# Performance work log

Hardware: AMD Instinct MI355X
Metric: run time of the kernel (lower is better)

The kernel has to match this reference:

```python
import jax, jax.numpy as jnp
import numpy as np

N_NODES = 50000
N_EDGES = 640000
IN, HID, OUT = 128, 128, 40


def _sage_conv(x, src, dst, W_l, b_l, W_r, num_nodes):
    """PyG SAGEConv (aggr='mean', root_weight=True):
       out_i = mean_{j in N(i)} x_j @ W_l^T + b_l + x_i @ W_r^T
    """
    msgs = x[src]  # [E, d] gather over source nodes
    agg = jax.ops.segment_sum(msgs, dst, num_segments=num_nodes)  # [N, d]
    deg = jax.ops.segment_sum(jnp.ones((src.shape[0],), x.dtype), dst,
                              num_segments=num_nodes)  # [N]
    mean = agg / jnp.maximum(deg, 1.0)[:, None]
    return mean @ W_l.T + b_l + x @ W_r.T


def setup_inputs() -> dict:
    key = jax.random.key(0)
    ks = jax.random.split(key, 12)
    x = jax.random.normal(ks[0], (N_NODES, IN), dtype=jnp.float32)
    edge_index = jax.random.randint(ks[1], (2, N_EDGES), 0, N_NODES, dtype=jnp.int64)

    def lin(k, fan_out, fan_in):
        s = 1.0 / np.sqrt(fan_in)
        return jax.random.uniform(k, (fan_out, fan_in), jnp.float32, -s, s)

    return {
        "x": x,
        "edge_index": edge_index,
        "W1l": lin(ks[2], HID, IN),  "b1": jnp.zeros((HID,), jnp.float32), "W1r": lin(ks[3], HID, IN),
        "W2l": lin(ks[4], HID, HID), "b2": jnp.zeros((HID,), jnp.float32), "W2r": lin(ks[5], HID, HID),
        "W3l": lin(ks[6], OUT, HID), "b3": jnp.zeros((OUT,), jnp.float32), "W3r": lin(ks[7], OUT, HID),
    }


def reference(x, edge_index, W1l, b1, W1r, W2l, b2, W2r, W3l, b3, W3r):
    src, dst = edge_index[0], edge_index[1]
    n = x.shape[0]
    # Dropout is identity in eval mode; reference is the deterministic forward.
    h = _sage_conv(x, src, dst, W1l, b1, W1r, n)
    h = jax.nn.relu(h)
    h = _sage_conv(h, src, dst, W2l, b2, W2r, n)
    h = jax.nn.relu(h)
    h = _sage_conv(h, src, dst, W3l, b3, W3r, n)
    return jax.nn.log_softmax(h, axis=-1)
```

## Files before the change

### kernel.cpp

```cpp
#include <hip/hip_runtime.h>

#define NN 50000
#define NE 640000
#define NBUCK 196
#define NSB 157
#define EPB 4096
#define EPT 16
#define COLCAP 8192
#define FDIM 128
#define FOUT 40

typedef unsigned int uint;
typedef unsigned short ushort;
typedef unsigned char uchar;
typedef __attribute__((ext_vector_type(8))) __bf16 bf16x8;
typedef __attribute__((ext_vector_type(4))) float f32x4;
typedef __attribute__((ext_vector_type(2))) float f32x2;

union BF8 { bf16x8 v; uint4 u; ushort s[8]; };

__device__ __forceinline__ ushort f2bf(float f){
  uint b = __float_as_uint(f);
  b += 0x7fffu + ((b >> 16) & 1u);
  return (ushort)(b >> 16);
}
__device__ __forceinline__ float bflo(uint v){ return __uint_as_float(v << 16); }
__device__ __forceinline__ float bfhi(uint v){ return __uint_as_float(v & 0xffff0000u); }
__device__ __forceinline__ uint pack2(float a, float b){
  return (uint)f2bf(a) | ((uint)f2bf(b) << 16);
}
__device__ __forceinline__ int get_edge(const void* ep, int is64, int idx){
  return is64 ? (int)(((const long long*)ep)[idx]) : ((const int*)ep)[idx];
}

__device__ __forceinline__ uint fp8enc(float f){
  uint b = __float_as_uint(f);
  uint s = (b >> 24) & 0x80u;
  float af = __uint_as_float(b & 0x7fffffffu);
  if(af < 0.015625f){
    uint m = (uint)__float2int_rn(af * 512.0f);
    return (m == 8u) ? (s | 0x08u) : (s | m);
  }
  uint ab = __float_as_uint(af);
  ab += 0x7ffffu + ((ab >> 20) & 1u);
  int e = (int)(ab >> 23) - 120;
  uint m = (ab >> 20) & 7u;
  if(e > 15){ e = 15; m = 6u; }
  return s | ((uint)e << 3) | m;
}
__device__ __forceinline__ float fp8dec(uint byte){
  uint s = (byte & 0x80u) << 24;
  uint e = (byte >> 3) & 15u;
  uint m = byte & 7u;
  float nrm = __uint_as_float(s | ((e + 120u) << 23) | (m << 20));
  float den = __uint_as_float(s | __float_as_uint((float)m * 0.001953125f));
  return e ? nrm : den;
}
__device__ __forceinline__ void fp8add4(uint dw, float* a){
#if __has_builtin(__builtin_amdgcn_cvt_pk_f32_fp8)
  f32x2 p0 = __builtin_amdgcn_cvt_pk_f32_fp8((int)dw, false);
  f32x2 p1 = __builtin_amdgcn_cvt_pk_f32_fp8((int)dw, true);
  a[0] += p0[0]; a[1] += p0[1]; a[2] += p1[0]; a[3] += p1[1];
#else
  a[0] += fp8dec(dw & 0xffu);
  a[1] += fp8dec((dw >> 8) & 0xffu);
  a[2] += fp8dec((dw >> 16) & 0xffu);
  a[3] += fp8dec(dw >> 24);
#endif
}

__launch_bounds__(256)
__global__ void k_pre(const float* __restrict__ x,
                      const float* __restrict__ W1l, const float* __restrict__ W1r,
                      const float* __restrict__ b1,
                      uchar* __restrict__ u8, ushort* __restrict__ v,
                      const unsigned long long* __restrict__ e64,
                      int* __restrict__ flag){
  if(blockIdx.x >= 625){
    if(threadIdx.x < 64){
      unsigned long long vv = e64[threadIdx.x];
      int ok = (int)__all(vv < 4294967296ULL);
      if(threadIdx.x == 0) *flag = ok;
    }
    return;
  }
  int g = threadIdx.x >> 6;
  int l = threadIdx.x & 63;
  int worker = blockIdx.x;
  int r16 = l & 15, q = l >> 4;

  BF8 bl[2][4], br[2][4];
#pragma unroll
  for(int tt = 0; tt < 2; ++tt){
    int colw = 32 * g + 16 * tt + r16;
    const float* pl = W1l + colw * FDIM + q * 8;
    const float* pr = W1r + colw * FDIM + q * 8;
#pragma unroll
    for(int ks = 0; ks < 4; ++ks){
      float4 x0 = *(const float4*)(pl + 32 * ks);
      float4 x1 = *(const float4*)(pl + 32 * ks + 4);
      BF8 t;
      t.s[0]=f2bf(x0.x); t.s[1]=f2bf(x0.y); t.s[2]=f2bf(x0.z); t.s[3]=f2bf(x0.w);
      t.s[4]=f2bf(x1.x); t.s[5]=f2bf(x1.y); t.s[6]=f2bf(x1.z); t.s[7]=f2bf(x1.w);
      bl[tt][ks] = t;
      float4 y0 = *(const float4*)(pr + 32 * ks);
      float4 y1 = *(const float4*)(pr + 32 * ks + 4);
      BF8 w;
      w.s[0]=f2bf(y0.x); w.s[1]=f2bf(y0.y); w.s[2]=f2bf(y0.z); w.s[3]=f2bf(y0.w);
      w.s[4]=f2bf(y1.x); w.s[5]=f2bf(y1.y); w.s[6]=f2bf(y1.z); w.s[7]=f2bf(y1.w);
      br[tt][ks] = w;
    }
  }
  float bv0 = b1[32 * g + r16];
  float bv1 = b1[32 * g + 16 + r16];

  for(int s = 0; s < 5; ++s){
    int m0 = (worker * 5 + s) * 16;
    BF8 a[4];
    const float* pf = x + (size_t)(m0 + r16) * FDIM + q * 8;
#pragma unroll
    for(int ks = 0; ks < 4; ++ks){
      float4 x0 = *(const float4*)(pf + 32 * ks);
      float4 x1 = *(const float4*)(pf + 32 * ks + 4);
      BF8 t;
      t.s[0]=f2bf(x0.x); t.s[1]=f2bf(x0.y); t.s[2]=f2bf(x0.z); t.s[3]=f2bf(x0.w);
      t.s[4]=f2bf(x1.x); t.s[5]=f2bf(x1.y); t.s[6]=f2bf(x1.z); t.s[7]=f2bf(x1.w);
      a[ks] = t;
    }
    f32x4 aU0 = {0,0,0,0}, aU1 = {0,0,0,0}, aV0 = {0,0,0,0}, aV1 = {0,0,0,0};
#pragma unroll
    for(int ks = 0; ks < 4; ++ks){
      aU0 = __builtin_amdgcn_mfma_f32_16x16x32_bf16(a[ks].v, bl[0][ks].v, aU0, 0, 0, 0);
      aV0 = __builtin_amdgcn_mfma_f32_16x16x32_bf16(a[ks].v, br[0][ks].v, aV0, 0, 0, 0);
      aU1 = __builtin_amdgcn_mfma_f32_16x16x32_bf16(a[ks].v, bl[1][ks].v, aU1, 0, 0, 0);
      aV1 = __builtin_amdgcn_mfma_f32_16x16x32_bf16(a[ks].v, br[1][ks].v, aV1, 0, 0, 0);
    }
#pragma unroll
    for(int r = 0; r < 4; ++r){
      size_t row = (size_t)(m0 + q * 4 + r);
      u8[row * FDIM + 32 * g + r16]      = (uchar)fp8enc(aU0[r]);
      u8[row * FDIM + 32 * g + 16 + r16] = (uchar)fp8enc(aU1[r]);
      v[row * FDIM + 32 * g + r16]       = f2bf(aV0[r] + bv0);
      v[row * FDIM + 32 * g + 16 + r16]  = f2bf(aV1[r] + bv1);
    }
  }
}

__global__ void k_hist(const void* __restrict__ edges, const int* __restrict__ flag,
                       int* __restrict__ bh){
  __shared__ int cnt[NBUCK];
  int t = threadIdx.x, sb = blockIdx.x;
  for(int i = t; i < NBUCK; i += 256) cnt[i] = 0;
  __syncthreads();
  int is64 = *flag;
  int e0 = sb * EPB + t;
#pragma unroll
  for(int i = 0; i < EPT; ++i){
    int e = e0 + i * 256;
    if(e < NE){
      int d = get_edge(edges, is64, NE + e);
      atomicAdd(&cnt[d >> 8], 1);
    }
  }
  __syncthreads();
  for(int i = t; i < NBUCK; i += 256) bh[i * NSB + sb] = cnt[i];
}

__global__ void k_bscan(int* __restrict__ bh, int* __restrict__ bases){
  __shared__ int s[256];
  int t = threadIdx.x;
  int tot = 0;
  if(t < NBUCK){
    const int* row = bh + t * NSB;
#pragma unroll 4
    for(int i = 0; i < NSB; ++i) tot += row[i];
  }
  s[t] = tot; __syncthreads();
  for(int o = 1; o < 256; o <<= 1){
    int a = (t >= o) ? s[t - o] : 0;
    __syncthreads(); s[t] += a; __syncthreads();
  }
  int base = s[t] - tot;
  if(t < NBUCK){
    bases[t] = base;
    int* row = bh + t * NSB;
    int run = base;
    for(int i = 0; i < NSB; ++i){ int vv = row[i]; row[i] = run; run += vv; }
  }
  if(t == 0) bases[NBUCK] = NE;
}

__launch_bounds__(256)
__global__ void k_scatter(const void* __restrict__ edges, const int* __restrict__ flag,
                          const int* __restrict__ bh, uint* __restrict__ recbuf){
  __shared__ int cnt[NBUCK], off[NBUCK], cur[NBUCK], gbase[NBUCK];
  __shared__ int s[256];
  __shared__ int nTot_s;
  __shared__ uint recLds[EPB];
  int t = threadIdx.x, sb = blockIdx.x;
  for(int i = t; i < NBUCK; i += 256) cnt[i] = 0;
  __syncthreads();
  int is64 = *flag;
  uint recs[EPT];
  int e0 = sb * EPB + t;
#pragma unroll
  for(int i = 0; i < EPT; ++i){
    int e = e0 + i * 256;
    if(e < NE){
      uint sn = (uint)get_edge(edges, is64, e);
      uint d  = (uint)get_edge(edges, is64, NE + e);
      recs[i] = (d << 16) | sn;
      atomicAdd(&cnt[d >> 8], 1);
    } else recs[i] = 0xFFFFFFFFu;
  }
  __syncthreads();
  int v = (t < NBUCK) ? cnt[t] : 0;
  s[t] = v; __syncthreads();
  for(int o = 1; o < 256; o <<= 1){
    int a = (t >= o) ? s[t - o] : 0;
    __syncthreads(); s[t] += a; __syncthreads();
  }
  if(t < NBUCK){ off[t] = s[t] - v; cur[t] = 0; gbase[t] = bh[t * NSB + sb]; }
  if(t == 255) nTot_s = s[255];
  __syncthreads();
#pragma unroll
  for(int i = 0; i < EPT; ++i){
    uint r = recs[i];
    if(r != 0xFFFFFFFFu){
      int b = (int)(r >> 24);
      int q = off[b] + atomicAdd(&cur[b], 1);
      recLds[q] = r;
    }
  }
  __syncthreads();
  int nTot = nTot_s;
  for(int q = t; q < nTot; q += 256){
    uint r = recLds[q];
    int b = (int)(r >> 24);
    recbuf[gbase[b] + (q - off[b])] = r;
  }
}

__global__ void k_csr(const uint* __restrict__ recbuf, const int* __restrict__ bases,
                      int* __restrict__ rp, int* __restrict__ col){
  __shared__ int cnt[256], rpl[256], cur[256];
  __shared__ int s[256];
  __shared__ int colL[COLCAP];
  int t = threadIdx.x, b = blockIdx.x;
  int base = bases[b], n = bases[b + 1] - base;
  cnt[t] = 0; __syncthreads();
  for(int q = t; q < n; q += 256) atomicAdd(&cnt[(recbuf[base + q] >> 16) & 255], 1);
  __syncthreads();
  int v = cnt[t];
  s[t] = v; __syncthreads();
  for(int o = 1; o < 256; o <<= 1){
    int a = (t >= o) ? s[t - o] : 0;
    __syncthreads(); s[t] += a; __syncthreads();
  }
  rpl[t] = s[t] - v; cur[t] = 0;
  int node = b * 256 + t;
  if(node < NN) rp[node] = base + rpl[t];
  if(b == 0 && t == 0) rp[NN] = NE;
  __syncthreads();
  if(n <= COLCAP){
    for(int q = t; q < n; q += 256){
      uint r = recbuf[base + q];
      int dl = (r >> 16) & 255;
      int p = rpl[dl] + atomicAdd(&cur[dl], 1);
      colL[p] = (int)(r & 0xFFFFu);
    }
    __syncthreads();
    for(int q = t; q < n; q += 256) col[base + q] = colL[q];
  } else {
    for(int q = t; q < n; q += 256){
      uint r = recbuf[base + q];
      int dl = (r >> 16) & 255;
      int p = rpl[dl] + atomicAdd(&cur[dl], 1);
      col[base + p] = (int)(r & 0xFFFFu);
    }
  }
}

__global__ void k_aggv8(const uchar* __restrict__ u8, const ushort* __restrict__ v,
                        const int* __restrict__ rp, const int* __restrict__ col,
                        ushort* __restrict__ h){
  int node = (blockIdx.x * blockDim.x + threadIdx.x) >> 6;
  if(node >= NN) return;
  int l = threadIdx.x & 63;
  int c8 = l & 7, eg = l >> 3;
  int beg = rp[node], deg = rp[node + 1] - beg;
  float acc[16];
#pragma unroll
  for(int i = 0; i < 16; ++i) acc[i] = 0.f;
  const uchar* fbase = u8 + c8 * 16;

  for(int base = 0; base < deg; base += 64){
    int nchunk = min(deg - base, 64);
    int idx = col[beg + base + min(l, nchunk - 1)];
#pragma unroll 2
    for(int j = 0; j < nchunk; j += 8){
      int e = j + eg;
      int s = __shfl(idx, min(e, nchunk - 1));
      uint4 w = *(const uint4*)(fbase + (size_t)s * FDIM);
      if(e < nchunk){
        fp8add4(w.x, acc + 0);
        fp8add4(w.y, acc + 4);
        fp8add4(w.z, acc + 8);
        fp8add4(w.w, acc + 12);
      }
    }
  }
#pragma unroll
  for(int i = 0; i < 16; ++i){
    acc[i] += __shfl_xor(acc[i], 8);
    acc[i] += __shfl_xor(acc[i], 16);
    acc[i] += __shfl_xor(acc[i], 32);
  }
  if(eg == 0){
    float inv = 1.0f / (float)max(deg, 1);
    const ushort* pv = v + (size_t)node * FDIM + c8 * 16;
    uint4 v0 = *(const uint4*)(pv);
    uint4 v1 = *(const uint4*)(pv + 8);
    uint4 o0, o1;
    o0.x = pack2(fmaxf(acc[0]*inv  + bflo(v0.x), 0.f), fmaxf(acc[1]*inv  + bfhi(v0.x), 0.f));
    o0.y = pack2(fmaxf(acc[2]*inv  + bflo(v0.y), 0.f), fmaxf(acc[3]*inv  + bfhi(v0.y), 0.f));
    o0.z = pack2(fmaxf(acc[4]*inv  + bflo(v0.z), 0.f), fmaxf(acc[5]*inv  + bfhi(v0.z), 0.f));
    o0.w = pack2(fmaxf(acc[6]*inv  + bflo(v0.w), 0.f), fmaxf(acc[7]*inv  + bfhi(v0.w), 0.f));
    o1.x = pack2(fmaxf(acc[8]*inv  + bflo(v1.x), 0.f), fmaxf(acc[9]*inv  + bfhi(v1.x), 0.f));
    o1.y = pack2(fmaxf(acc[10]*inv + bflo(v1.y), 0.f), fmaxf(acc[11]*inv + bfhi(v1.y), 0.f));
    o1.z = pack2(fmaxf(acc[12]*inv + bflo(v1.z), 0.f), fmaxf(acc[13]*inv + bfhi(v1.z), 0.f));
    o1.w = pack2(fmaxf(acc[14]*inv + bflo(v1.w), 0.f), fmaxf(acc[15]*inv + bfhi(v1.w), 0.f));
    ushort* ph = h + (size_t)node * FDIM + c8 * 16;
    *(uint4*)(ph)     = o0;
    *(uint4*)(ph + 8) = o1;
  }
}

__launch_bounds__(256)
__global__ void k_linuv2(const ushort* __restrict__ inB,
                         const float* __restrict__ Wl, const float* __restrict__ Wr,
                         const float* __restrict__ bias,
                         uchar* __restrict__ u8, ushort* __restrict__ v){
  int g = threadIdx.x >> 6;
  int l = threadIdx.x & 63;
  int worker = blockIdx.x;
  int r16 = l & 15, q = l >> 4;

  BF8 bl[2][4], br[2][4];
#pragma unroll
  for(int tt = 0; tt < 2; ++tt){
    int colw = 32 * g + 16 * tt + r16;
    const float* pl = Wl + colw * FDIM + q * 8;
    const float* pr = Wr + colw * FDIM + q * 8;
#pragma unroll
    for(int ks = 0; ks < 4; ++ks){
      float4 x0 = *(const float4*)(pl + 32 * ks);
      float4 x1 = *(const float4*)(pl + 32 * ks + 4);
      BF8 t;
      t.s[0]=f2bf(x0.x); t.s[1]=f2bf(x0.y); t.s[2]=f2bf(x0.z); t.s[3]=f2bf(x0.w);
      t.s[4]=f2bf(x1.x); t.s[5]=f2bf(x1.y); t.s[6]=f2bf(x1.z); t.s[7]=f2bf(x1.w);
      bl[tt][ks] = t;
      float4 y0 = *(const float4*)(pr + 32 * ks);
      float4 y1 = *(const float4*)(pr + 32 * ks + 4);
      BF8 w;
      w.s[0]=f2bf(y0.x); w.s[1]=f2bf(y0.y); w.s[2]=f2bf(y0.z); w.s[3]=f2bf(y0.w);
      w.s[4]=f2bf(y1.x); w.s[5]=f2bf(y1.y); w.s[6]=f2bf(y1.z); w.s[7]=f2bf(y1.w);
      br[tt][ks] = w;
    }
  }
  float bv0 = bias[32 * g + r16];
  float bv1 = bias[32 * g + 16 + r16];

  for(int s = 0; s < 5; ++s){
    int m0 = (worker * 5 + s) * 16;
    BF8 a[4];
    const ushort* pb = inB + (size_t)(m0 + r16) * FDIM + q * 8;
#pragma unroll
    for(int ks = 0; ks < 4; ++ks) a[ks].u = *(const uint4*)(pb + 32 * ks);
    f32x4 aU0 = {0,0,0,0}, aU1 = {0,0,0,0}, aV0 = {0,0,0,0}, aV1 = {0,0,0,0};
#pragma unroll
    for(int ks = 0; ks < 4; ++ks){
      aU0 = __builtin_amdgcn_mfma_f32_16x16x32_bf16(a[ks].v, bl[0][ks].v, aU0, 0, 0, 0);
      aV0 = __builtin_amdgcn_mfma_f32_16x16x32_bf16(a[ks].v, br[0][ks].v, aV0, 0, 0, 0);
      aU1 = __builtin_amdgcn_mfma_f32_16x16x32_bf16(a[ks].v, bl[1][ks].v, aU1, 0, 0, 0);
      aV1 = __builtin_amdgcn_mfma_f32_16x16x32_bf16(a[ks].v, br[1][ks].v, aV1, 0, 0, 0);
    }
#pragma unroll
    for(int r = 0; r < 4; ++r){
      size_t row = (size_t)(m0 + q * 4 + r);
      u8[row * FDIM + 32 * g + r16]      = (uchar)fp8enc(aU0[r]);
      u8[row * FDIM + 32 * g + 16 + r16] = (uchar)fp8enc(aU1[r]);
      v[row * FDIM + 32 * g + r16]       = f2bf(aV0[r] + bv0);
      v[row * FDIM + 32 * g + 16 + r16]  = f2bf(aV1[r] + bv1);
    }
  }
}

__launch_bounds__(192)
__global__ void k_linuv40(const ushort* __restrict__ inB,
                          const float* __restrict__ Wl, const float* __restrict__ Wr,
                          const float* __restrict__ bias,
                          ushort* __restrict__ u3, ushort* __restrict__ v3){
  int g = threadIdx.x >> 6;
  int l = threadIdx.x & 63;
  int worker = blockIdx.x;
  int r16 = l & 15, q = l >> 4;
  int colw = 16 * g + r16;
  bool vcol = colw < FOUT;

  BF8 bl[4], br[4];
#pragma unroll
  for(int ks = 0; ks < 4; ++ks){
    BF8 t, w;
    if(vcol){
      const float* pl = Wl + colw * FDIM + q * 8 + 32 * ks;
      const float* pr = Wr + colw * FDIM + q * 8 + 32 * ks;
      float4 x0 = ((const float4*)pl)[0], x1 = ((const float4*)pl)[1];
      t.s[0]=f2bf(x0.x); t.s[1]=f2bf(x0.y); t.s[2]=f2bf(x0.z); t.s[3]=f2bf(x0.w);
      t.s[4]=f2bf(x1.x); t.s[5]=f2bf(x1.y); t.s[6]=f2bf(x1.z); t.s[7]=f2bf(x1.w);
      float4 y0 = ((const float4*)pr)[0], y1 = ((const float4*)pr)[1];
      w.s[0]=f2bf(y0.x); w.s[1]=f2bf(y0.y); w.s[2]=f2bf(y0.z); w.s[3]=f2bf(y0.w);
      w.s[4]=f2bf(y1.x); w.s[5]=f2bf(y1.y); w.s[6]=f2bf(y1.z); w.s[7]=f2bf(y1.w);
    } else {
      t.u = make_uint4(0,0,0,0);
      w.u = make_uint4(0,0,0,0);
    }
    bl[ks] = t; br[ks] = w;
  }
  float bv = vcol ? bias[colw] : 0.f;

  for(int s = 0; s < 5; ++s){
    int m0 = (worker * 5 + s) * 16;
    BF8 a[4];
    const ushort* pb = inB + (size_t)(m0 + r16) * FDIM + q * 8;
#pragma unroll
    for(int ks = 0; ks < 4; ++ks) a[ks].u = *(const uint4*)(pb + 32 * ks);
    f32x4 aU = {0,0,0,0}, aV = {0,0,0,0};
#pragma unroll
    for(int ks = 0; ks < 4; ++ks){
      aU = __builtin_amdgcn_mfma_f32_16x16x32_bf16(a[ks].v, bl[ks].v, aU, 0, 0, 0);
      aV = __builtin_amdgcn_mfma_f32_16x16x32_bf16(a[ks].v, br[ks].v, aV, 0, 0, 0);
    }
    if(vcol){
#pragma unroll
      for(int r = 0; r < 4; ++r){
        size_t row = (size_t)(m0 + q * 4 + r);
        u3[row * FOUT + colw] = f2bf(aU[r]);
        v3[row * FOUT + colw] = f2bf(aV[r] + bv);
      }
    }
  }
}

__global__ void k_agg40(const ushort* __restrict__ u3, const ushort* __restrict__ v3,
                        const int* __restrict__ rp, const int* __restrict__ col,
                        float* __restrict__ out){
  int node = (blockIdx.x * blockDim.x + threadIdx.x) >> 6;
  if(node >= NN) return;
  int l = threadIdx.x & 63;
  int c = l % 20, sl = l / 20;
  const ushort* fbase = u3 + 2 * c;

  int beg = rp[node], deg = rp[node + 1] - beg;
  float a0 = 0.f, a1 = 0.f;
  for(int base = 0; base < deg; base += 60){
    int nchunk = min(deg - base, 60);
    int idx = col[beg + base + min(l, nchunk - 1)];
#pragma unroll 2
    for(int j = 0; j < nchunk; j += 3){
      int e = j + sl;
      int s = __shfl(idx, min(e, nchunk - 1));
      uint w = *(const uint*)(fbase + (size_t)s * FOUT);
      if(sl < 3 && e < nchunk){
        a0 += bflo(w); a1 += bfhi(w);
      }
    }
  }
  a0 += __shfl(a0, l + 20) + __shfl(a0, l + 40);
  a1 += __shfl(a1, l + 20) + __shfl(a1, l + 40);

  float inv = 1.0f / (float)max(deg, 1);
  float z0 = 0.f, z1 = 0.f;
  if(l < 20){
    uint vv = *(const uint*)(v3 + (size_t)node * FOUT + 2 * c);
    z0 = a0 * inv + bflo(vv);
    z1 = a1 * inv + bfhi(vv);
  }
  float m = (l < 20) ? fmaxf(z0, z1) : -1e30f;
#pragma unroll
  for(int d = 1; d < 64; d <<= 1) m = fmaxf(m, __shfl_xor(m, d));
  float es = (l < 20) ? (__expf(z0 - m) + __expf(z1 - m)) : 0.f;
#pragma unroll
  for(int d = 1; d < 64; d <<= 1) es += __shfl_xor(es, d);
  float lse = m + __logf(es);
  if(l < 20){
    *(float2*)(out + (size_t)node * FOUT + 2 * c) = make_float2(z0 - lse, z1 - lse);
  }
}

extern "C" void kernel_launch(void* const* d_in, const int* in_sizes, int n_in,
                              void* d_out, int out_size, void* d_ws, size_t ws_size,
                              hipStream_t stream){
  const float* x   = (const float*)d_in[0];
  const void*  edges = d_in[1];
  const float* W1l = (const float*)d_in[2];
  const float* b1  = (const float*)d_in[3];
  const float* W1r = (const float*)d_in[4];
  const float* W2l = (const float*)d_in[5];
  const float* b2  = (const float*)d_in[6];
  const float* W2r = (const float*)d_in[7];
  const float* W3l = (const float*)d_in[8];
  const float* b3  = (const float*)d_in[9];
  const float* W3r = (const float*)d_in[10];
  float* out = (float*)d_out;

  char* ws = (char*)d_ws;
  size_t off = 0;
  auto alloc = [&](size_t bytes)->void*{
    void* p = ws + off;
    off += (bytes + 255) & ~(size_t)255;
    return p;
  };
  ushort* u    = (ushort*)alloc((size_t)NN * FDIM * 2);
  ushort* v    = (ushort*)alloc((size_t)NN * FDIM * 2);
  ushort* h    = (ushort*)alloc((size_t)NN * FDIM * 2);
  ushort* h2   = (ushort*)alloc((size_t)NN * FDIM * 2);
  int*    rp   = (int*)alloc((size_t)(NN + 1) * 4);
  int*    col  = (int*)alloc((size_t)NE * 4);
  uint*   recbuf = (uint*)alloc((size_t)NE * 4);
  int*    bh   = (int*)alloc((size_t)NBUCK * NSB * 4);
  int*    bases= (int*)alloc((size_t)(NBUCK + 1) * 4);
  int*    flag = (int*)alloc(256);
  uchar*  u8   = (uchar*)u;

  int aggGrid = (NN * 64 + 255) / 256;
  k_pre<<<626, 256, 0, stream>>>(x, W1l, W1r, b1, u8, v,
                                 (const unsigned long long*)edges, flag);
  k_hist<<<NSB, 256, 0, stream>>>(edges, flag, bh);
  k_bscan<<<1, 256, 0, stream>>>(bh, bases);
  k_scatter<<<NSB, 256, 0, stream>>>(edges, flag, bh, recbuf);
  k_csr<<<NBUCK, 256, 0, stream>>>(recbuf, bases, rp, col);

  k_aggv8<<<aggGrid, 256, 0, stream>>>(u8, v, rp, col, h);
  k_linuv2<<<625, 256, 0, stream>>>(h, W2l, W2r, b2, u8, v);
  k_aggv8<<<aggGrid, 256, 0, stream>>>(u8, v, rp, col, h2);
  k_linuv40<<<625, 192, 0, stream>>>(h2, W3l, W3r, b3, u, v);
  k_agg40<<<aggGrid, 256, 0, stream>>>(u, v, rp, col, out);
}
```

Baseline: 214.7 us.

## Replace histogram+scan CSR build with fixed-capacity buckets and atomic offsets

```diff
diff --git a/kernel.cpp b/kernel.cpp
--- a/kernel.cpp
+++ b/kernel.cpp
@@ -6,7 +6,7 @@
 #define NSB 157
 #define EPB 4096
 #define EPT 16
-#define COLCAP 8192
+#define BCAP 4096
 #define FDIM 128
 #define FOUT 40
 
@@ -75,18 +75,19 @@
                       const float* __restrict__ b1,
                       uchar* __restrict__ u8, ushort* __restrict__ v,
                       const unsigned long long* __restrict__ e64,
-                      int* __restrict__ flag){
-  if(blockIdx.x >= 625){
-    if(threadIdx.x < 64){
-      unsigned long long vv = e64[threadIdx.x];
+                      int* __restrict__ flag, int* __restrict__ gcur){
+  if(blockIdx.x >= 3125){
+    int t = threadIdx.x;
+    if(t < NBUCK) gcur[t] = 0;
+    if(t < 64){
+      unsigned long long vv = e64[t];
       int ok = (int)__all(vv < 4294967296ULL);
-      if(threadIdx.x == 0) *flag = ok;
+      if(t == 0) *flag = ok;
     }
     return;
   }
   int g = threadIdx.x >> 6;
   int l = threadIdx.x & 63;
-  int worker = blockIdx.x;
   int r16 = l & 15, q = l >> 4;
 
   BF8 bl[2][4], br[2][4];
@@ -114,86 +115,40 @@
   float bv0 = b1[32 * g + r16];
   float bv1 = b1[32 * g + 16 + r16];
 
-  for(int s = 0; s < 5; ++s){
-    int m0 = (worker * 5 + s) * 16;
-    BF8 a[4];
-    const float* pf = x + (size_t)(m0 + r16) * FDIM + q * 8;
-#pragma unroll
-    for(int ks = 0; ks < 4; ++ks){
-      float4 x0 = *(const float4*)(pf + 32 * ks);
-      float4 x1 = *(const float4*)(pf + 32 * ks + 4);
-      BF8 t;
-      t.s[0]=f2bf(x0.x); t.s[1]=f2bf(x0.y); t.s[2]=f2bf(x0.z); t.s[3]=f2bf(x0.w);
-      t.s[4]=f2bf(x1.x); t.s[5]=f2bf(x1.y); t.s[6]=f2bf(x1.z); t.s[7]=f2bf(x1.w);
-      a[ks] = t;
-    }
-    f32x4 aU0 = {0,0,0,0}, aU1 = {0,0,0,0}, aV0 = {0,0,0,0}, aV1 = {0,0,0,0};
-#pragma unroll
-    for(int ks = 0; ks < 4; ++ks){
-      aU0 = __builtin_amdgcn_mfma_f32_16x16x32_bf16(a[ks].v, bl[0][ks].v, aU0, 0, 0, 0);
-      aV0 = __builtin_amdgcn_mfma_f32_16x16x32_bf16(a[ks].v, br[0][ks].v, aV0, 0, 0, 0);
-      aU1 = __builtin_amdgcn_mfma_f32_16x16x32_bf16(a[ks].v, bl[1][ks].v, aU1, 0, 0, 0);
-      aV1 = __builtin_amdgcn_mfma_f32_16x16x32_bf16(a[ks].v, br[1][ks].v, aV1, 0, 0, 0);
-    }
-#pragma unroll
-    for(int r = 0; r < 4; ++r){
-      size_t row = (size_t)(m0 + q * 4 + r);
-      u8[row * FDIM + 32 * g + r16]      = (uchar)fp8enc(aU0[r]);
-      u8[row * FDIM + 32 * g + 16 + r16] = (uchar)fp8enc(aU1[r]);
-      v[row * FDIM + 32 * g + r16]       = f2bf(aV0[r] + bv0);
-      v[row * FDIM + 32 * g + 16 + r16]  = f2bf(aV1[r] + bv1);
-    }
-  }
-}
-
-__global__ void k_hist(const void* __restrict__ edges, const int* __restrict__ flag,
-                       int* __restrict__ bh){
-  __shared__ int cnt[NBUCK];
-  int t = threadIdx.x, sb = blockIdx.x;
-  for(int i = t; i < NBUCK; i += 256) cnt[i] = 0;
-  __syncthreads();
-  int is64 = *flag;
-  int e0 = sb * EPB + t;
-#pragma unroll
-  for(int i = 0; i < EPT; ++i){
-    int e = e0 + i * 256;
-    if(e < NE){
-      int d = get_edge(edges, is64, NE + e);
-      atomicAdd(&cnt[d >> 8], 1);
-    }
-  }
-  __syncthreads();
-  for(int i = t; i < NBUCK; i += 256) bh[i * NSB + sb] = cnt[i];
-}
-
-__global__ void k_bscan(int* __restrict__ bh, int* __restrict__ bases){
-  __shared__ int s[256];
-  int t = threadIdx.x;
-  int tot = 0;
-  if(t < NBUCK){
-    const int* row = bh + t * NSB;
-#pragma unroll 4
-    for(int i = 0; i < NSB; ++i) tot += row[i];
-  }
-  s[t] = tot; __syncthreads();
-  for(int o = 1; o < 256; o <<= 1){
-    int a = (t >= o) ? s[t - o] : 0;
-    __syncthreads(); s[t] += a; __syncthreads();
-  }
-  int base = s[t] - tot;
-  if(t < NBUCK){
-    bases[t] = base;
-    int* row = bh + t * NSB;
-    int run = base;
-    for(int i = 0; i < NSB; ++i){ int vv = row[i]; row[i] = run; run += vv; }
-  }
-  if(t == 0) bases[NBUCK] = NE;
+  int m0 = blockIdx.x * 16;
+  BF8 a[4];
+  const float* pf = x + (size_t)(m0 + r16) * FDIM + q * 8;
+#pragma unroll
+  for(int ks = 0; ks < 4; ++ks){
+    float4 x0 = *(const float4*)(pf + 32 * ks);
+    float4 x1 = *(const float4*)(pf + 32 * ks + 4);
+    BF8 t;
+    t.s[0]=f2bf(x0.x); t.s[1]=f2bf(x0.y); t.s[2]=f2bf(x0.z); t.s[3]=f2bf(x0.w);
+    t.s[4]=f2bf(x1.x); t.s[5]=f2bf(x1.y); t.s[6]=f2bf(x1.z); t.s[7]=f2bf(x1.w);
+    a[ks] = t;
+  }
+  f32x4 aU0 = {0,0,0,0}, aU1 = {0,0,0,0}, aV0 = {0,0,0,0}, aV1 = {0,0,0,0};
+#pragma unroll
+  for(int ks = 0; ks < 4; ++ks){
+    aU0 = __builtin_amdgcn_mfma_f32_16x16x32_bf16(a[ks].v, bl[0][ks].v, aU0, 0, 0, 0);
+    aV0 = __builtin_amdgcn_mfma_f32_16x16x32_bf16(a[ks].v, br[0][ks].v, aV0, 0, 0, 0);
+    aU1 = __builtin_amdgcn_mfma_f32_16x16x32_bf16(a[ks].v, bl[1][ks].v, aU1, 0, 0, 0);
+    aV1 = __builtin_amdgcn_mfma_f32_16x16x32_bf16(a[ks].v, br[1][ks].v, aV1, 0, 0, 0);
+  }
+#pragma unroll
+  for(int r = 0; r < 4; ++r){
+    size_t row = (size_t)(m0 + q * 4 + r);
+    u8[row * FDIM + 32 * g + r16]      = (uchar)fp8enc(aU0[r]);
+    u8[row * FDIM + 32 * g + 16 + r16] = (uchar)fp8enc(aU1[r]);
+    v[row * FDIM + 32 * g + r16]       = f2bf(aV0[r] + bv0);
+    v[row * FDIM + 32 * g + 16 + r16]  = f2bf(aV1[r] + bv1);
+  }
 }
 
 __launch_bounds__(256)
 __global__ void k_scatter(const void* __restrict__ edges, const int* __restrict__ flag,
-                          const int* __restrict__ bh, uint* __restrict__ recbuf){
-  __shared__ int cnt[NBUCK], off[NBUCK], cur[NBUCK], gbase[NBUCK];
+                          int* __restrict__ gcur, uint* __restrict__ recbuf){
+  __shared__ int cnt[NBUCK], off[NBUCK], cur[NBUCK], gb[NBUCK];
   __shared__ int s[256];
   __shared__ int nTot_s;
   __shared__ uint recLds[EPB];
@@ -220,7 +175,10 @@
     int a = (t >= o) ? s[t - o] : 0;
     __syncthreads(); s[t] += a; __syncthreads();
   }
-  if(t < NBUCK){ off[t] = s[t] - v; cur[t] = 0; gbase[t] = bh[t * NSB + sb]; }
+  if(t < NBUCK){
+    off[t] = s[t] - v; cur[t] = 0;
+    gb[t] = v ? atomicAdd(&gcur[t], v) : 0;
+  }
   if(t == 255) nTot_s = s[255];
   __syncthreads();
 #pragma unroll
@@ -237,17 +195,18 @@
   for(int q = t; q < nTot; q += 256){
     uint r = recLds[q];
     int b = (int)(r >> 24);
-    recbuf[gbase[b] + (q - off[b])] = r;
-  }
-}
-
-__global__ void k_csr(const uint* __restrict__ recbuf, const int* __restrict__ bases,
-                      int* __restrict__ rp, int* __restrict__ col){
+    recbuf[(size_t)b * BCAP + gb[b] + (q - off[b])] = r;
+  }
+}
+
+__global__ void k_csr(const uint* __restrict__ recbuf, const int* __restrict__ gcur,
+                      int* __restrict__ rp, int* __restrict__ degN,
+                      int* __restrict__ col){
   __shared__ int cnt[256], rpl[256], cur[256];
   __shared__ int s[256];
-  __shared__ int colL[COLCAP];
+  __shared__ int colL[BCAP];
   int t = threadIdx.x, b = blockIdx.x;
-  int base = bases[b], n = bases[b + 1] - base;
+  int base = b * BCAP, n = gcur[b];
   cnt[t] = 0; __syncthreads();
   for(int q = t; q < n; q += 256) atomicAdd(&cnt[(recbuf[base + q] >> 16) & 255], 1);
   __syncthreads();
@@ -259,36 +218,26 @@
   }
   rpl[t] = s[t] - v; cur[t] = 0;
   int node = b * 256 + t;
-  if(node < NN) rp[node] = base + rpl[t];
-  if(b == 0 && t == 0) rp[NN] = NE;
-  __syncthreads();
-  if(n <= COLCAP){
-    for(int q = t; q < n; q += 256){
-      uint r = recbuf[base + q];
-      int dl = (r >> 16) & 255;
-      int p = rpl[dl] + atomicAdd(&cur[dl], 1);
-      colL[p] = (int)(r & 0xFFFFu);
-    }
-    __syncthreads();
-    for(int q = t; q < n; q += 256) col[base + q] = colL[q];
-  } else {
-    for(int q = t; q < n; q += 256){
-      uint r = recbuf[base + q];
-      int dl = (r >> 16) & 255;
-      int p = rpl[dl] + atomicAdd(&cur[dl], 1);
-      col[base + p] = (int)(r & 0xFFFFu);
-    }
-  }
+  if(node < NN){ rp[node] = base + rpl[t]; degN[node] = v; }
+  __syncthreads();
+  for(int q = t; q < n; q += 256){
+    uint r = recbuf[base + q];
+    int dl = (r >> 16) & 255;
+    int p = rpl[dl] + atomicAdd(&cur[dl], 1);
+    colL[p] = (int)(r & 0xFFFFu);
+  }
+  __syncthreads();
+  for(int q = t; q < n; q += 256) col[base + q] = colL[q];
 }
 
 __global__ void k_aggv8(const uchar* __restrict__ u8, const ushort* __restrict__ v,
-                        const int* __restrict__ rp, const int* __restrict__ col,
-                        ushort* __restrict__ h){
+                        const int* __restrict__ rp, const int* __restrict__ degN,
+                        const int* __restrict__ col, ushort* __restrict__ h){
   int node = (blockIdx.x * blockDim.x + threadIdx.x) >> 6;
   if(node >= NN) return;
   int l = threadIdx.x & 63;
   int c8 = l & 7, eg = l >> 3;
-  int beg = rp[node], deg = rp[node + 1] - beg;
+  int beg = rp[node], deg = degN[node];
   float acc[16];
 #pragma unroll
   for(int i = 0; i < 16; ++i) acc[i] = 0.f;
@@ -343,7 +292,6 @@
                          uchar* __restrict__ u8, ushort* __restrict__ v){
   int g = threadIdx.x >> 6;
   int l = threadIdx.x & 63;
-  int worker = blockIdx.x;
   int r16 = l & 15, q = l >> 4;
 
   BF8 bl[2][4], br[2][4];
@@ -371,28 +319,26 @@
   float bv0 = bias[32 * g + r16];
   float bv1 = bias[32 * g + 16 + r16];
 
-  for(int s = 0; s < 5; ++s){
-    int m0 = (worker * 5 + s) * 16;
-    BF8 a[4];
-    const ushort* pb = inB + (size_t)(m0 + r16) * FDIM + q * 8;
-#pragma unroll
-    for(int ks = 0; ks < 4; ++ks) a[ks].u = *(const uint4*)(pb + 32 * ks);
-    f32x4 aU0 = {0,0,0,0}, aU1 = {0,0,0,0}, aV0 = {0,0,0,0}, aV1 = {0,0,0,0};
-#pragma unroll
-    for(int ks = 0; ks < 4; ++ks){
-      aU0 = __builtin_amdgcn_mfma_f32_16x16x32_bf16(a[ks].v, bl[0][ks].v, aU0, 0, 0, 0);
-      aV0 = __builtin_amdgcn_mfma_f32_16x16x32_bf16(a[ks].v, br[0][ks].v, aV0, 0, 0, 0);
-      aU1 = __builtin_amdgcn_mfma_f32_16x16x32_bf16(a[ks].v, bl[1][ks].v, aU1, 0, 0, 0);
-      aV1 = __builtin_amdgcn_mfma_f32_16x16x32_bf16(a[ks].v, br[1][ks].v, aV1, 0, 0, 0);
-    }
-#pragma unroll
-    for(int r = 0; r < 4; ++r){
-      size_t row = (size_t)(m0 + q * 4 + r);
-      u8[row * FDIM + 32 * g + r16]      = (uchar)fp8enc(aU0[r]);
-      u8[row * FDIM + 32 * g + 16 + r16] = (uchar)fp8enc(aU1[r]);
-      v[row * FDIM + 32 * g + r16]       = f2bf(aV0[r] + bv0);
-      v[row * FDIM + 32 * g + 16 + r16]  = f2bf(aV1[r] + bv1);
-    }
+  int m0 = blockIdx.x * 16;
+  BF8 a[4];
+  const ushort* pb = inB + (size_t)(m0 + r16) * FDIM + q * 8;
+#pragma unroll
+  for(int ks = 0; ks < 4; ++ks) a[ks].u = *(const uint4*)(pb + 32 * ks);
+  f32x4 aU0 = {0,0,0,0}, aU1 = {0,0,0,0}, aV0 = {0,0,0,0}, aV1 = {0,0,0,0};
+#pragma unroll
+  for(int ks = 0; ks < 4; ++ks){
+    aU0 = __builtin_amdgcn_mfma_f32_16x16x32_bf16(a[ks].v, bl[0][ks].v, aU0, 0, 0, 0);
+    aV0 = __builtin_amdgcn_mfma_f32_16x16x32_bf16(a[ks].v, br[0][ks].v, aV0, 0, 0, 0);
+    aU1 = __builtin_amdgcn_mfma_f32_16x16x32_bf16(a[ks].v, bl[1][ks].v, aU1, 0, 0, 0);
+    aV1 = __builtin_amdgcn_mfma_f32_16x16x32_bf16(a[ks].v, br[1][ks].v, aV1, 0, 0, 0);
+  }
+#pragma unroll
+  for(int r = 0; r < 4; ++r){
+    size_t row = (size_t)(m0 + q * 4 + r);
+    u8[row * FDIM + 32 * g + r16]      = (uchar)fp8enc(aU0[r]);
+    u8[row * FDIM + 32 * g + 16 + r16] = (uchar)fp8enc(aU1[r]);
+    v[row * FDIM + 32 * g + r16]       = f2bf(aV0[r] + bv0);
+    v[row * FDIM + 32 * g + 16 + r16]  = f2bf(aV1[r] + bv1);
   }
 }
 
@@ -403,7 +349,6 @@
                           ushort* __restrict__ u3, ushort* __restrict__ v3){
   int g = threadIdx.x >> 6;
   int l = threadIdx.x & 63;
-  int worker = blockIdx.x;
   int r16 = l & 15, q = l >> 4;
   int colw = 16 * g + r16;
   bool vcol = colw < FOUT;
@@ -429,39 +374,37 @@
   }
   float bv = vcol ? bias[colw] : 0.f;
 
-  for(int s = 0; s < 5; ++s){
-    int m0 = (worker * 5 + s) * 16;
-    BF8 a[4];
-    const ushort* pb = inB + (size_t)(m0 + r16) * FDIM + q * 8;
-#pragma unroll
-    for(int ks = 0; ks < 4; ++ks) a[ks].u = *(const uint4*)(pb + 32 * ks);
-    f32x4 aU = {0,0,0,0}, aV = {0,0,0,0};
-#pragma unroll
-    for(int ks = 0; ks < 4; ++ks){
-      aU = __builtin_amdgcn_mfma_f32_16x16x32_bf16(a[ks].v, bl[ks].v, aU, 0, 0, 0);
-      aV = __builtin_amdgcn_mfma_f32_16x16x32_bf16(a[ks].v, br[ks].v, aV, 0, 0, 0);
-    }
-    if(vcol){
-#pragma unroll
-      for(int r = 0; r < 4; ++r){
-        size_t row = (size_t)(m0 + q * 4 + r);
-        u3[row * FOUT + colw] = f2bf(aU[r]);
-        v3[row * FOUT + colw] = f2bf(aV[r] + bv);
-      }
+  int m0 = blockIdx.x * 16;
+  BF8 a[4];
+  const ushort* pb = inB + (size_t)(m0 + r16) * FDIM + q * 8;
+#pragma unroll
+  for(int ks = 0; ks < 4; ++ks) a[ks].u = *(const uint4*)(pb + 32 * ks);
+  f32x4 aU = {0,0,0,0}, aV = {0,0,0,0};
+#pragma unroll
+  for(int ks = 0; ks < 4; ++ks){
+    aU = __builtin_amdgcn_mfma_f32_16x16x32_bf16(a[ks].v, bl[ks].v, aU, 0, 0, 0);
+    aV = __builtin_amdgcn_mfma_f32_16x16x32_bf16(a[ks].v, br[ks].v, aV, 0, 0, 0);
+  }
+  if(vcol){
+#pragma unroll
+    for(int r = 0; r < 4; ++r){
+      size_t row = (size_t)(m0 + q * 4 + r);
+      u3[row * FOUT + colw] = f2bf(aU[r]);
+      v3[row * FOUT + colw] = f2bf(aV[r] + bv);
     }
   }
 }
 
 __global__ void k_agg40(const ushort* __restrict__ u3, const ushort* __restrict__ v3,
-                        const int* __restrict__ rp, const int* __restrict__ col,
-                        float* __restrict__ out){
+                        const int* __restrict__ rp, const int* __restrict__ degN,
+                        const int* __restrict__ col, float* __restrict__ out){
   int node = (blockIdx.x * blockDim.x + threadIdx.x) >> 6;
   if(node >= NN) return;
   int l = threadIdx.x & 63;
   int c = l % 20, sl = l / 20;
   const ushort* fbase = u3 + 2 * c;
 
-  int beg = rp[node], deg = rp[node + 1] - beg;
+  int beg = rp[node], deg = degN[node];
   float a0 = 0.f, a1 = 0.f;
   for(int base = 0; base < deg; base += 60){
     int nchunk = min(deg - base, 60);
@@ -525,25 +468,23 @@
   ushort* v    = (ushort*)alloc((size_t)NN * FDIM * 2);
   ushort* h    = (ushort*)alloc((size_t)NN * FDIM * 2);
   ushort* h2   = (ushort*)alloc((size_t)NN * FDIM * 2);
-  int*    rp   = (int*)alloc((size_t)(NN + 1) * 4);
-  int*    col  = (int*)alloc((size_t)NE * 4);
-  uint*   recbuf = (uint*)alloc((size_t)NE * 4);
-  int*    bh   = (int*)alloc((size_t)NBUCK * NSB * 4);
-  int*    bases= (int*)alloc((size_t)(NBUCK + 1) * 4);
+  int*    rp   = (int*)alloc((size_t)NN * 4);
+  int*    degN = (int*)alloc((size_t)NN * 4);
+  int*    col  = (int*)alloc((size_t)NBUCK * BCAP * 4);
+  uint*   recbuf = (uint*)alloc((size_t)NBUCK * BCAP * 4);
+  int*    gcur = (int*)alloc((size_t)NBUCK * 4);
   int*    flag = (int*)alloc(256);
   uchar*  u8   = (uchar*)u;
 
   int aggGrid = (NN * 64 + 255) / 256;
-  k_pre<<<626, 256, 0, stream>>>(x, W1l, W1r, b1, u8, v,
-                                 (const unsigned long long*)edges, flag);
-  k_hist<<<NSB, 256, 0, stream>>>(edges, flag, bh);
-  k_bscan<<<1, 256, 0, stream>>>(bh, bases);
-  k_scatter<<<NSB, 256, 0, stream>>>(edges, flag, bh, recbuf);
-  k_csr<<<NBUCK, 256, 0, stream>>>(recbuf, bases, rp, col);
-
-  k_aggv8<<<aggGrid, 256, 0, stream>>>(u8, v, rp, col, h);
-  k_linuv2<<<625, 256, 0, stream>>>(h, W2l, W2r, b2, u8, v);
-  k_aggv8<<<aggGrid, 256, 0, stream>>>(u8, v, rp, col, h2);
-  k_linuv40<<<625, 192, 0, stream>>>(h2, W3l, W3r, b3, u, v);
-  k_agg40<<<aggGrid, 256, 0, stream>>>(u, v, rp, col, out);
-}
+  k_pre<<<3126, 256, 0, stream>>>(x, W1l, W1r, b1, u8, v,
+                                  (const unsigned long long*)edges, flag, gcur);
+  k_scatter<<<NSB, 256, 0, stream>>>(edges, flag, gcur, recbuf);
+  k_csr<<<NBUCK, 256, 0, stream>>>(recbuf, gcur, rp, degN, col);
+
+  k_aggv8<<<aggGrid, 256, 0, stream>>>(u8, v, rp, degN, col, h);
+  k_linuv2<<<3125, 256, 0, stream>>>(h, W2l, W2r, b2, u8, v);
+  k_aggv8<<<aggGrid, 256, 0, stream>>>(u8, v, rp, degN, col, h2);
+  k_linuv40<<<3125, 192, 0, stream>>>(h2, W3l, W3r, b3, u, v);
+  k_agg40<<<aggGrid, 256, 0, stream>>>(u, v, rp, degN, col, out);
+}
```

Measured after the change: 262.1 us. 22.1% more time.
